# Kernel optimization log

Hardware: AMD Instinct MI355X
Metric: run time of the kernel (lower is better)

Reference implementation:

```python
import jax, jax.numpy as jnp
from jax import lax
import numpy as np

B, T, E, H = 64, 512, 1024, 1024

def setup_inputs() -> dict:
    key = jax.random.key(0)
    k1, k2, k3, k4, k5, k6 = jax.random.split(key, 6)
    s = 1.0 / np.sqrt(H)  # torch LSTM init scale
    embeddings = jax.random.normal(k1, (B, T, E), dtype=jnp.float32)
    seq_lengths = jax.random.randint(k2, (B,), 1, T + 1)
    W_ih = jax.random.uniform(k3, (4 * H, E), minval=-s, maxval=s, dtype=jnp.float32)
    W_hh = jax.random.uniform(k4, (4 * H, H), minval=-s, maxval=s, dtype=jnp.float32)
    b_ih = jax.random.uniform(k5, (4 * H,), minval=-s, maxval=s, dtype=jnp.float32)
    b_hh = jax.random.uniform(k6, (4 * H,), minval=-s, maxval=s, dtype=jnp.float32)
    return {"embeddings": embeddings, "seq_lengths": seq_lengths,
            "W_ih": W_ih, "W_hh": W_hh, "b_ih": b_ih, "b_hh": b_hh}

def _lstm_outputs(embeddings, W_ih, W_hh, b_ih, b_hh):
    x = jnp.swapaxes(embeddings, 0, 1)  # [T, B, E] (time-major, as nn.LSTM batch_first=False)
    # Hoist the input projection into one big GEMM: [T,B,4H]
    x_proj = jnp.einsum('tbe,ge->tbg', x, W_ih) + b_ih + b_hh

    def step(carry, xp):
        h, c = carry
        gates = xp + h @ W_hh.T                      # [B, 4H]
        i, f, g, o = jnp.split(gates, 4, axis=-1)    # torch gate order: i, f, g, o
        i = jax.nn.sigmoid(i)
        f = jax.nn.sigmoid(f)
        g = jnp.tanh(g)
        o = jax.nn.sigmoid(o)
        c = f * c + i * g
        h = o * jnp.tanh(c)
        return (h, c), h

    h0 = jnp.zeros((x.shape[1], W_hh.shape[1]), x.dtype)
    _, outs = lax.scan(step, (h0, h0), x_proj)       # outs: [T, B, H]
    return outs

def reference(embeddings, seq_lengths, W_ih, W_hh, b_ih, b_hh):
    outs = _lstm_outputs(embeddings, W_ih, W_hh, b_ih, b_hh)  # [T, B, H]
    t = outs.shape[0]
    idx = (seq_lengths - 1) % t                      # wraps like python negative indexing
    repr_ = outs[idx, jnp.arange(outs.shape[1])]     # [B, H]
    return repr_
```

## Files before the change

kernel.cpp:

```cpp
#include <hip/hip_runtime.h>
#include <stdint.h>


typedef _Float16 half8 __attribute__((ext_vector_type(8)));
typedef _Float16 half4_ __attribute__((ext_vector_type(4)));
typedef float f32x4 __attribute__((ext_vector_type(4)));
typedef unsigned int u32x4 __attribute__((ext_vector_type(4)));

#define T_SEQ 512

__global__ void k_f32_to_f16(const float* __restrict__ s, _Float16* __restrict__ d, int n4) {
  int i = blockIdx.x * blockDim.x + threadIdx.x;
  if (i >= n4) return;
  f32x4 v = ((const f32x4*)s)[i];
  half4_ h;
  h.x = (_Float16)v.x; h.y = (_Float16)v.y; h.z = (_Float16)v.z; h.w = (_Float16)v.w;
  ((half4_*)d)[i] = h;
}

__global__ void k_bias_sum(const float* __restrict__ a, const float* __restrict__ b,
                           float* __restrict__ o) {
  int i = blockIdx.x * blockDim.x + threadIdx.x;
  if (i < 4096) o[i] = a[i] + b[i];
}

__global__ __launch_bounds__(256, 2) void k_gemm_xproj(
    const _Float16* __restrict__ X, const _Float16* __restrict__ W,
    const float* __restrict__ bsum, _Float16* __restrict__ C) {
  __shared__ _Float16 As[128 * 64];
  __shared__ _Float16 Bs[128 * 64];
  const int bid = blockIdx.x;
  const int ntile = bid & 31, mtile = bid >> 5;
  const int tid = threadIdx.x;
  const int wave = tid >> 6, lane = tid & 63;
  const int wr = wave >> 1, wc = wave & 1;
  const int R0 = lane >> 3, cg = lane & 7;

  f32x4 acc[4][4];
#pragma unroll
  for (int m = 0; m < 4; m++)
#pragma unroll
    for (int n = 0; n < 4; n++) acc[m][n] = (f32x4){0.f, 0.f, 0.f, 0.f};

  for (int k0 = 0; k0 < 1024; k0 += 64) {
#pragma unroll
    for (int i = 0; i < 4; i++) {
      const int rr = (wave * 4 + i) * 8 + R0;
      const _Float16* ga = X + (size_t)(mtile * 128 + rr) * 1024 + k0 + ((cg ^ (rr & 7)) * 8);
      const _Float16* gb = W + (size_t)(ntile * 128 + rr) * 1024 + k0 + ((cg ^ (rr & 7)) * 8);
      __builtin_amdgcn_global_load_lds(
          (const __attribute__((address_space(1))) void*)ga,
          (__attribute__((address_space(3))) void*)((char*)As + (wave * 4 + i) * 1024), 16, 0, 0);
      __builtin_amdgcn_global_load_lds(
          (const __attribute__((address_space(1))) void*)gb,
          (__attribute__((address_space(3))) void*)((char*)Bs + (wave * 4 + i) * 1024), 16, 0, 0);
    }
    asm volatile("s_waitcnt vmcnt(0)" ::: "memory");
    __syncthreads();
#pragma unroll
    for (int kk = 0; kk < 2; kk++) {
      half8 af[4], bf[4];
#pragma unroll
      for (int m = 0; m < 4; m++) {
        int r = wr * 64 + m * 16 + (lane & 15);
        af[m] = *(const half8*)((const char*)As + r * 128 +
                                (((kk * 4 + (lane >> 4)) ^ (r & 7)) << 4));
      }
#pragma unroll
      for (int n = 0; n < 4; n++) {
        int r = wc * 64 + n * 16 + (lane & 15);
        bf[n] = *(const half8*)((const char*)Bs + r * 128 +
                                (((kk * 4 + (lane >> 4)) ^ (r & 7)) << 4));
      }
#pragma unroll
      for (int m = 0; m < 4; m++)
#pragma unroll
        for (int n = 0; n < 4; n++)
          acc[m][n] = __builtin_amdgcn_mfma_f32_16x16x32_f16(af[m], bf[n], acc[m][n], 0, 0, 0);
    }
    __syncthreads();
  }
#pragma unroll
  for (int n = 0; n < 4; n++) {
    int col = ntile * 128 + wc * 64 + n * 16 + (lane & 15);
    float bs = bsum[col];
#pragma unroll
    for (int m = 0; m < 4; m++)
#pragma unroll
      for (int q = 0; q < 4; q++) {
        int row = mtile * 128 + wr * 64 + m * 16 + (lane >> 4) * 4 + q;
        int bb = row >> 9, tt = row & 511;
        C[((size_t)tt * 64 + bb) * 4096 + col] = (_Float16)(acc[m][n][q] + bs);
      }
  }
}

__global__ __launch_bounds__(256, 1) void k_lstm_rec(
    const _Float16* __restrict__ Whh,
    const _Float16* __restrict__ xprojT,
    const int* __restrict__ seqlen,
    unsigned* __restrict__ hbuf,
    float* __restrict__ out) {
  __shared__ _Float16 h_lds[16 * 1024];
  __shared__ float gates[64 * 17];

  const int bid = blockIdx.x;
  const int x8 = bid & 7;
  const int g = x8 >> 1;
  const int s = (x8 & 1) * 32 + (bid >> 3);
  const int tid = threadIdx.x;
  const int wave = tid >> 6, lane = tid & 63;

  for (int i = tid; i < 4096; i += 256) ((uint64_t*)h_lds)[i] = 0ull;

  half8 wfrag[32];
  {
    const _Float16* wp =
        Whh + (size_t)(1024 * wave + s * 16 + (lane & 15)) * 1024 + (lane >> 4) * 8;
#pragma unroll
    for (int kk = 0; kk < 32; kk++) wfrag[kk] = *(const half8*)(wp + kk * 32);
  }

  int Lg = 1;
  for (int b = 0; b < 16; b++) {
    int L = seqlen[g * 16 + b];
    Lg = L > Lg ? L : Lg;
  }
  const int be = tid >> 4, ue = tid & 15;
  const int mylen = seqlen[g * 16 + be];
  float c_state = 0.f;

  const int rowbase = (lane & 15) * 2048;
  const int xorm = ((lane & 15) & 7) << 4;

  __syncthreads();

  for (int t = 0; t < Lg; t++) {
    float xp[4];
#pragma unroll
    for (int q = 0; q < 4; q++) {
      int bm = (lane >> 4) * 4 + q;
      xp[q] = (float)xprojT[((size_t)t * 64 + g * 16 + bm) * 4096 + 1024 * wave + s * 16 +
                            (lane & 15)];
    }

    if (t > 0) {
      const unsigned* src = hbuf + ((size_t)(t & 1)) * 65536 + (size_t)g * 16384;
      const unsigned Etag = (unsigned)t << 16;
#pragma unroll
      for (int hf = 0; hf < 2; hf++) {
        u32x4 hv[8];
        unsigned done = 0;
        while (done != 0xFFu) {
#pragma unroll
          for (int i = 0; i < 8; i++) {
            if (!(done & (1u << i))) {
              asm volatile("global_load_dwordx4 %0, %1, off sc0 sc1"
                           : "=v"(hv[i])
                           : "v"(src + (size_t)(tid + ((hf * 8 + i) << 8)) * 4)
                           : "memory");
            }
          }
          asm volatile("s_waitcnt vmcnt(0)" ::: "memory");
#pragma unroll
          for (int i = 0; i < 8; i++) {
            if (!(done & (1u << i))) {
              unsigned m = ((hv[i].x ^ Etag) | (hv[i].y ^ Etag) | (hv[i].z ^ Etag) |
                            (hv[i].w ^ Etag)) & 0xFFFF0000u;
              if (__all(m == 0u)) done |= 1u << i;
            }
          }
        }
#pragma unroll
        for (int i = 0; i < 8; i++) {
          int ch = tid + ((hf * 8 + i) << 8);
          int br = ch >> 8, cidx = ch & 255;
          unsigned lo = (hv[i].x & 0xFFFFu) | (hv[i].y << 16);
          unsigned hi = (hv[i].z & 0xFFFFu) | (hv[i].w << 16);
          *(uint64_t*)((char*)h_lds + br * 2048 + (((cidx >> 1) ^ (br & 7)) << 4) +
                       (cidx & 1) * 8) = (uint64_t)lo | ((uint64_t)hi << 32);
        }
      }
    }
    __syncthreads();

    f32x4 a0 = (f32x4){0.f, 0.f, 0.f, 0.f};
    f32x4 a1 = (f32x4){0.f, 0.f, 0.f, 0.f};
    f32x4 a2 = (f32x4){0.f, 0.f, 0.f, 0.f};
    f32x4 a3 = (f32x4){0.f, 0.f, 0.f, 0.f};
    const char* lb = (const char*)h_lds + rowbase;
#pragma unroll
    for (int kk = 0; kk < 32; kk += 4) {
      half8 f0 = *(const half8*)(lb + ((((kk + 0) * 4 + (lane >> 4)) << 4) ^ xorm));
      half8 f1 = *(const half8*)(lb + ((((kk + 1) * 4 + (lane >> 4)) << 4) ^ xorm));
      half8 f2 = *(const half8*)(lb + ((((kk + 2) * 4 + (lane >> 4)) << 4) ^ xorm));
      half8 f3 = *(const half8*)(lb + ((((kk + 3) * 4 + (lane >> 4)) << 4) ^ xorm));
      a0 = __builtin_amdgcn_mfma_f32_16x16x32_f16(f0, wfrag[kk + 0], a0, 0, 0, 0);
      a1 = __builtin_amdgcn_mfma_f32_16x16x32_f16(f1, wfrag[kk + 1], a1, 0, 0, 0);
      a2 = __builtin_amdgcn_mfma_f32_16x16x32_f16(f2, wfrag[kk + 2], a2, 0, 0, 0);
      a3 = __builtin_amdgcn_mfma_f32_16x16x32_f16(f3, wfrag[kk + 3], a3, 0, 0, 0);
    }
    {
      f32x4 gv4;
#pragma unroll
      for (int q = 0; q < 4; q++) gv4[q] = (a0[q] + a1[q]) + (a2[q] + a3[q]) + xp[q];
      *(f32x4*)&gates[(wave * 16 + (lane & 15)) * 17 + (lane >> 4) * 4] = gv4;
    }
    __syncthreads();

    float iv = gates[(0 + ue) * 17 + be];
    float fv = gates[(16 + ue) * 17 + be];
    float gv = gates[(32 + ue) * 17 + be];
    float ov = gates[(48 + ue) * 17 + be];
    iv = 1.f / (1.f + __expf(-iv));
    fv = 1.f / (1.f + __expf(-fv));
    gv = 1.f - 2.f / (1.f + __expf(2.f * gv));
    ov = 1.f / (1.f + __expf(-ov));
    c_state = fv * c_state + iv * gv;
    float tc = 1.f - 2.f / (1.f + __expf(2.f * c_state));
    float hv = ov * tc;
    if (t + 1 == mylen) out[(size_t)(g * 16 + be) * 1024 + s * 16 + ue] = hv;

    if (t + 1 < Lg) {
      _Float16 hfv = (_Float16)hv;
      unsigned short hb;
      __builtin_memcpy(&hb, &hfv, 2);
      unsigned tw = ((unsigned)(t + 1) << 16) | (unsigned)hb;
      __hip_atomic_store(hbuf + ((size_t)((t + 1) & 1)) * 65536 +
                             (size_t)(g * 16 + be) * 1024 + s * 16 + ue,
                         tw, __ATOMIC_RELAXED, __HIP_MEMORY_SCOPE_AGENT);
    }
  }
}

extern "C" void kernel_launch(void* const* d_in, const int* in_sizes, int n_in, void* d_out,
                              int out_size, void* d_ws, size_t ws_size, hipStream_t stream) {
  const float* emb = (const float*)d_in[0];
  const int* slen = (const int*)d_in[1];
  const float* Wih = (const float*)d_in[2];
  const float* Whh = (const float*)d_in[3];
  const float* bih = (const float*)d_in[4];
  const float* bhh = (const float*)d_in[5];
  float* out = (float*)d_out;

  char* ws = (char*)d_ws;
  _Float16* xprojT = (_Float16*)(ws + 0);
  _Float16* xf = (_Float16*)(ws + 268435456);
  unsigned* hbuf = (unsigned*)(ws + 268435456);
  _Float16* wihf = (_Float16*)(ws + 335544320);
  _Float16* whhf = (_Float16*)(ws + 343932928);
  float* bsum = (float*)(ws + 352321536);

  k_f32_to_f16<<<(8388608 + 255) / 256, 256, 0, stream>>>(emb, xf, 8388608);
  k_f32_to_f16<<<(1048576 + 255) / 256, 256, 0, stream>>>(Wih, wihf, 1048576);
  k_f32_to_f16<<<(1048576 + 255) / 256, 256, 0, stream>>>(Whh, whhf, 1048576);
  k_bias_sum<<<16, 256, 0, stream>>>(bih, bhh, bsum);
  k_gemm_xproj<<<8192, 256, 0, stream>>>(xf, wihf, bsum, xprojT);
  hipMemsetAsync(hbuf, 0, 524288, stream);
  k_lstm_rec<<<256, 256, 0, stream>>>(whhf, xprojT, slen, hbuf, out);
}
```

Baseline: 1.947 ms.

## Fuse input projection into recurrent LSTM kernel with overlapped per-step staging

Drops the separate x-projection GEMM kernel and its large fp16 intermediate buffer. The recurrent kernel now keeps W_ih fragments in registers alongside W_hh. It stages each next timestep's embeddings into double-buffered LDS with global_load_lds, then computes that step's input projection via MFMA after publishing h, so the work overlaps the cross-block wait. This removes the big GEMM and its memory traffic, and it also skips projection work for timesteps beyond each group's max length. The cost is doubled register pressure (64 half8 fragments per lane), more LDS, and extra MFMA work placed on the serial recurrence path.

```diff
diff --git a/kernel.cpp b/kernel.cpp
--- a/kernel.cpp
+++ b/kernel.cpp
@@ -6,8 +6,6 @@
 typedef _Float16 half4_ __attribute__((ext_vector_type(4)));
 typedef float f32x4 __attribute__((ext_vector_type(4)));
 typedef unsigned int u32x4 __attribute__((ext_vector_type(4)));
-
-#define T_SEQ 512
 
 __global__ void k_f32_to_f16(const float* __restrict__ s, _Float16* __restrict__ d, int n4) {
   int i = blockIdx.x * blockDim.x + threadIdx.x;
@@ -24,84 +22,16 @@
   if (i < 4096) o[i] = a[i] + b[i];
 }
 
-__global__ __launch_bounds__(256, 2) void k_gemm_xproj(
-    const _Float16* __restrict__ X, const _Float16* __restrict__ W,
-    const float* __restrict__ bsum, _Float16* __restrict__ C) {
-  __shared__ _Float16 As[128 * 64];
-  __shared__ _Float16 Bs[128 * 64];
-  const int bid = blockIdx.x;
-  const int ntile = bid & 31, mtile = bid >> 5;
-  const int tid = threadIdx.x;
-  const int wave = tid >> 6, lane = tid & 63;
-  const int wr = wave >> 1, wc = wave & 1;
-  const int R0 = lane >> 3, cg = lane & 7;
-
-  f32x4 acc[4][4];
-#pragma unroll
-  for (int m = 0; m < 4; m++)
-#pragma unroll
-    for (int n = 0; n < 4; n++) acc[m][n] = (f32x4){0.f, 0.f, 0.f, 0.f};
-
-  for (int k0 = 0; k0 < 1024; k0 += 64) {
-#pragma unroll
-    for (int i = 0; i < 4; i++) {
-      const int rr = (wave * 4 + i) * 8 + R0;
-      const _Float16* ga = X + (size_t)(mtile * 128 + rr) * 1024 + k0 + ((cg ^ (rr & 7)) * 8);
-      const _Float16* gb = W + (size_t)(ntile * 128 + rr) * 1024 + k0 + ((cg ^ (rr & 7)) * 8);
-      __builtin_amdgcn_global_load_lds(
-          (const __attribute__((address_space(1))) void*)ga,
-          (__attribute__((address_space(3))) void*)((char*)As + (wave * 4 + i) * 1024), 16, 0, 0);
-      __builtin_amdgcn_global_load_lds(
-          (const __attribute__((address_space(1))) void*)gb,
-          (__attribute__((address_space(3))) void*)((char*)Bs + (wave * 4 + i) * 1024), 16, 0, 0);
-    }
-    asm volatile("s_waitcnt vmcnt(0)" ::: "memory");
-    __syncthreads();
-#pragma unroll
-    for (int kk = 0; kk < 2; kk++) {
-      half8 af[4], bf[4];
-#pragma unroll
-      for (int m = 0; m < 4; m++) {
-        int r = wr * 64 + m * 16 + (lane & 15);
-        af[m] = *(const half8*)((const char*)As + r * 128 +
-                                (((kk * 4 + (lane >> 4)) ^ (r & 7)) << 4));
-      }
-#pragma unroll
-      for (int n = 0; n < 4; n++) {
-        int r = wc * 64 + n * 16 + (lane & 15);
-        bf[n] = *(const half8*)((const char*)Bs + r * 128 +
-                                (((kk * 4 + (lane >> 4)) ^ (r & 7)) << 4));
-      }
-#pragma unroll
-      for (int m = 0; m < 4; m++)
-#pragma unroll
-        for (int n = 0; n < 4; n++)
-          acc[m][n] = __builtin_amdgcn_mfma_f32_16x16x32_f16(af[m], bf[n], acc[m][n], 0, 0, 0);
-    }
-    __syncthreads();
-  }
-#pragma unroll
-  for (int n = 0; n < 4; n++) {
-    int col = ntile * 128 + wc * 64 + n * 16 + (lane & 15);
-    float bs = bsum[col];
-#pragma unroll
-    for (int m = 0; m < 4; m++)
-#pragma unroll
-      for (int q = 0; q < 4; q++) {
-        int row = mtile * 128 + wr * 64 + m * 16 + (lane >> 4) * 4 + q;
-        int bb = row >> 9, tt = row & 511;
-        C[((size_t)tt * 64 + bb) * 4096 + col] = (_Float16)(acc[m][n][q] + bs);
-      }
-  }
-}
-
 __global__ __launch_bounds__(256, 1) void k_lstm_rec(
     const _Float16* __restrict__ Whh,
-    const _Float16* __restrict__ xprojT,
+    const _Float16* __restrict__ Wih,
+    const _Float16* __restrict__ xf,
+    const float* __restrict__ bsum,
     const int* __restrict__ seqlen,
     unsigned* __restrict__ hbuf,
     float* __restrict__ out) {
   __shared__ _Float16 h_lds[16 * 1024];
+  __shared__ _Float16 axf[2][16 * 1024];
   __shared__ float gates[64 * 17];
 
   const int bid = blockIdx.x;
@@ -113,13 +43,18 @@
 
   for (int i = tid; i < 4096; i += 256) ((uint64_t*)h_lds)[i] = 0ull;
 
-  half8 wfrag[32];
+  half8 wfhh[32], wfih[32];
   {
-    const _Float16* wp =
-        Whh + (size_t)(1024 * wave + s * 16 + (lane & 15)) * 1024 + (lane >> 4) * 8;
-#pragma unroll
-    for (int kk = 0; kk < 32; kk++) wfrag[kk] = *(const half8*)(wp + kk * 32);
+    const size_t roff = (size_t)(1024 * wave + s * 16 + (lane & 15)) * 1024 + (lane >> 4) * 8;
+    const _Float16* ph = Whh + roff;
+    const _Float16* pi = Wih + roff;
+#pragma unroll
+    for (int kk = 0; kk < 32; kk++) {
+      wfhh[kk] = *(const half8*)(ph + kk * 32);
+      wfih[kk] = *(const half8*)(pi + kk * 32);
+    }
   }
+  const float bs = bsum[1024 * wave + s * 16 + (lane & 15)];
 
   int Lg = 1;
   for (int b = 0; b < 16; b++) {
@@ -133,16 +68,49 @@
   const int rowbase = (lane & 15) * 2048;
   const int xorm = ((lane & 15) & 7) << 4;
 
+  auto STAGE = [&](int tt) {
+    const int bufsel = tt & 1;
+#pragma unroll
+    for (int i = 0; i < 8; i++) {
+      const int ch = tid + (i << 8);
+      const int br = ch >> 7, cidx = ch & 127;
+      const _Float16* gp =
+          xf + ((size_t)(g * 16 + br) * 512 + tt) * 1024 + ((cidx ^ (br & 7)) * 8);
+      __builtin_amdgcn_global_load_lds(
+          (const __attribute__((address_space(1))) void*)gp,
+          (__attribute__((address_space(3))) void*)((char*)axf[bufsel] +
+                                                    ((wave * 64 + (i << 8)) << 4)),
+          16, 0, 0);
+    }
+  };
+
+  f32x4 xa0, xa1, xa2, xa3;
+  auto XP_COMPUTE = [&](int tt) {
+    xa0 = (f32x4){bs, bs, bs, bs};
+    xa1 = (f32x4){0.f, 0.f, 0.f, 0.f};
+    xa2 = (f32x4){0.f, 0.f, 0.f, 0.f};
+    xa3 = (f32x4){0.f, 0.f, 0.f, 0.f};
+    const char* ab = (const char*)axf[tt & 1] + rowbase;
+#pragma unroll
+    for (int kk = 0; kk < 32; kk += 4) {
+      half8 f0 = *(const half8*)(ab + ((((kk + 0) * 4 + (lane >> 4)) << 4) ^ xorm));
+      half8 f1 = *(const half8*)(ab + ((((kk + 1) * 4 + (lane >> 4)) << 4) ^ xorm));
+      half8 f2 = *(const half8*)(ab + ((((kk + 2) * 4 + (lane >> 4)) << 4) ^ xorm));
+      half8 f3 = *(const half8*)(ab + ((((kk + 3) * 4 + (lane >> 4)) << 4) ^ xorm));
+      xa0 = __builtin_amdgcn_mfma_f32_16x16x32_f16(f0, wfih[kk + 0], xa0, 0, 0, 0);
+      xa1 = __builtin_amdgcn_mfma_f32_16x16x32_f16(f1, wfih[kk + 1], xa1, 0, 0, 0);
+      xa2 = __builtin_amdgcn_mfma_f32_16x16x32_f16(f2, wfih[kk + 2], xa2, 0, 0, 0);
+      xa3 = __builtin_amdgcn_mfma_f32_16x16x32_f16(f3, wfih[kk + 3], xa3, 0, 0, 0);
+    }
+  };
+
+  STAGE(0);
+  asm volatile("s_waitcnt vmcnt(0)" ::: "memory");
   __syncthreads();
+  XP_COMPUTE(0);
 
   for (int t = 0; t < Lg; t++) {
-    float xp[4];
-#pragma unroll
-    for (int q = 0; q < 4; q++) {
-      int bm = (lane >> 4) * 4 + q;
-      xp[q] = (float)xprojT[((size_t)t * 64 + g * 16 + bm) * 4096 + 1024 * wave + s * 16 +
-                            (lane & 15)];
-    }
+    if (t + 1 < Lg) STAGE(t + 1);
 
     if (t > 0) {
       const unsigned* src = hbuf + ((size_t)(t & 1)) * 65536 + (size_t)g * 16384;
@@ -184,10 +152,7 @@
     }
     __syncthreads();
 
-    f32x4 a0 = (f32x4){0.f, 0.f, 0.f, 0.f};
-    f32x4 a1 = (f32x4){0.f, 0.f, 0.f, 0.f};
-    f32x4 a2 = (f32x4){0.f, 0.f, 0.f, 0.f};
-    f32x4 a3 = (f32x4){0.f, 0.f, 0.f, 0.f};
+    f32x4 a0 = xa0, a1 = xa1, a2 = xa2, a3 = xa3;
     const char* lb = (const char*)h_lds + rowbase;
 #pragma unroll
     for (int kk = 0; kk < 32; kk += 4) {
@@ -195,15 +160,15 @@
       half8 f1 = *(const half8*)(lb + ((((kk + 1) * 4 + (lane >> 4)) << 4) ^ xorm));
       half8 f2 = *(const half8*)(lb + ((((kk + 2) * 4 + (lane >> 4)) << 4) ^ xorm));
       half8 f3 = *(const half8*)(lb + ((((kk + 3) * 4 + (lane >> 4)) << 4) ^ xorm));
-      a0 = __builtin_amdgcn_mfma_f32_16x16x32_f16(f0, wfrag[kk + 0], a0, 0, 0, 0);
-      a1 = __builtin_amdgcn_mfma_f32_16x16x32_f16(f1, wfrag[kk + 1], a1, 0, 0, 0);
-      a2 = __builtin_amdgcn_mfma_f32_16x16x32_f16(f2, wfrag[kk + 2], a2, 0, 0, 0);
-      a3 = __builtin_amdgcn_mfma_f32_16x16x32_f16(f3, wfrag[kk + 3], a3, 0, 0, 0);
+      a0 = __builtin_amdgcn_mfma_f32_16x16x32_f16(f0, wfhh[kk + 0], a0, 0, 0, 0);
+      a1 = __builtin_amdgcn_mfma_f32_16x16x32_f16(f1, wfhh[kk + 1], a1, 0, 0, 0);
+      a2 = __builtin_amdgcn_mfma_f32_16x16x32_f16(f2, wfhh[kk + 2], a2, 0, 0, 0);
+      a3 = __builtin_amdgcn_mfma_f32_16x16x32_f16(f3, wfhh[kk + 3], a3, 0, 0, 0);
     }
     {
       f32x4 gv4;
 #pragma unroll
-      for (int q = 0; q < 4; q++) gv4[q] = (a0[q] + a1[q]) + (a2[q] + a3[q]) + xp[q];
+      for (int q = 0; q < 4; q++) gv4[q] = (a0[q] + a1[q]) + (a2[q] + a3[q]);
       *(f32x4*)&gates[(wave * 16 + (lane & 15)) * 17 + (lane >> 4) * 4] = gv4;
     }
     __syncthreads();
@@ -222,13 +187,15 @@
     if (t + 1 == mylen) out[(size_t)(g * 16 + be) * 1024 + s * 16 + ue] = hv;
 
     if (t + 1 < Lg) {
-      _Float16 hfv = (_Float16)hv;
+      _Float16 hf16 = (_Float16)hv;
       unsigned short hb;
-      __builtin_memcpy(&hb, &hfv, 2);
+      __builtin_memcpy(&hb, &hf16, 2);
       unsigned tw = ((unsigned)(t + 1) << 16) | (unsigned)hb;
       __hip_atomic_store(hbuf + ((size_t)((t + 1) & 1)) * 65536 +
                              (size_t)(g * 16 + be) * 1024 + s * 16 + ue,
                          tw, __ATOMIC_RELAXED, __HIP_MEMORY_SCOPE_AGENT);
+
+      XP_COMPUTE(t + 1);
     }
   }
 }
@@ -244,18 +211,16 @@
   float* out = (float*)d_out;
 
   char* ws = (char*)d_ws;
-  _Float16* xprojT = (_Float16*)(ws + 0);
-  _Float16* xf = (_Float16*)(ws + 268435456);
-  unsigned* hbuf = (unsigned*)(ws + 268435456);
-  _Float16* wihf = (_Float16*)(ws + 335544320);
-  _Float16* whhf = (_Float16*)(ws + 343932928);
-  float* bsum = (float*)(ws + 352321536);
+  _Float16* xf = (_Float16*)(ws + 0);
+  _Float16* wihf = (_Float16*)(ws + 67108864);
+  _Float16* whhf = (_Float16*)(ws + 75497472);
+  float* bsum = (float*)(ws + 83886080);
+  unsigned* hbuf = (unsigned*)(ws + 83902464);
 
   k_f32_to_f16<<<(8388608 + 255) / 256, 256, 0, stream>>>(emb, xf, 8388608);
   k_f32_to_f16<<<(1048576 + 255) / 256, 256, 0, stream>>>(Wih, wihf, 1048576);
   k_f32_to_f16<<<(1048576 + 255) / 256, 256, 0, stream>>>(Whh, whhf, 1048576);
   k_bias_sum<<<16, 256, 0, stream>>>(bih, bhh, bsum);
-  k_gemm_xproj<<<8192, 256, 0, stream>>>(xf, wihf, bsum, xprojT);
   hipMemsetAsync(hbuf, 0, 524288, stream);
-  k_lstm_rec<<<256, 256, 0, stream>>>(whhf, xprojT, slen, hbuf, out);
-}
+  k_lstm_rec<<<256, 256, 0, stream>>>(whhf, wihf, xf, bsum, slen, hbuf, out);
+}
```

New measurement: 2.098 ms. +7.8%, slower.
